# Kernel optimization log

Measured on AMD Instinct MI355X. Metric: run time of the kernel, lower is better.

Reference implementation:

```python
import jax, jax.numpy as jnp
import numpy as np

B, L, C = 16, 4000, 512
W = 5            # window_size == reduction
NH_G = 4         # int(8 * 0.5) grid-attention heads
NH_P = 4         # 8 - 4 pool-attention heads
DG = 256         # int(C * 0.5) grid inner dim
DP = 256         # int(C * (1 - 0.5)) pool inner dim
HD = 64          # head dim for both branches
EPS = 1e-5       # LayerNorm eps (torch default)


def setup_inputs() -> dict:
    key = jax.random.key(0)
    ks = jax.random.split(key, 8)
    s = 0.02
    return {
        "x": jax.random.normal(ks[0], (B, L, C), jnp.float32),
        # all linear weights stored [in, out] (torch Linear does x @ W.T)
        "gqkv_w": jax.random.normal(ks[1], (C, 3 * DG), jnp.float32) * s,
        "gqkv_b": jnp.zeros((3 * DG,), jnp.float32),
        "pq_w": jax.random.normal(ks[2], (C, DP), jnp.float32) * s,
        "pq_b": jnp.zeros((DP,), jnp.float32),
        "pkv_w": jax.random.normal(ks[3], (C, 2 * DP), jnp.float32) * s,
        "pkv_b": jnp.zeros((2 * DP,), jnp.float32),
        "conv_w": jax.random.normal(ks[4], (C, C), jnp.float32) * s,  # 1x1 Conv1d
        "conv_b": jnp.zeros((C,), jnp.float32),
        "ln_g": jnp.ones((C,), jnp.float32),
        "ln_b": jnp.zeros((C,), jnp.float32),
        "proj_w": jax.random.normal(ks[5], (C, C), jnp.float32) * s,
        "proj_b": jnp.zeros((C,), jnp.float32),
    }


def _mhsa(q, k, v, scale):
    # q,k,v: [b, h, n, hd]
    attn = jax.nn.softmax(jnp.einsum('bhqd,bhkd->bhqk', q, k) * scale, axis=-1)
    return jnp.einsum('bhqk,bhkd->bhqd', attn, v)


def reference(x, gqkv_w, gqkv_b, pq_w, pq_b, pkv_w, pkv_b,
              conv_w, conv_b, ln_g, ln_b, proj_w, proj_b):
    b, l, c = x.shape
    n = l // W
    scale = HD ** -0.5

    # ---- GridAttention (strided-window attention, ratio=0.5) ----
    # unfold: [b, l, c] -> [b*W, n, c] grouping tokens by residue mod W
    xg = x.reshape(b, n, W, c).transpose(0, 2, 1, 3).reshape(b * W, n, c)
    qkv = (xg @ gqkv_w + gqkv_b).reshape(b * W, n, 3, NH_G, HD).transpose(2, 0, 3, 1, 4)
    og = _mhsa(qkv[0], qkv[1], qkv[2], scale)               # [b*W, h, n, hd]
    og = og.transpose(0, 2, 1, 3).reshape(b, W, n, DG)       # back to [b, W, n, DG]
    og = og.transpose(0, 2, 1, 3).reshape(b, l, DG)          # fold -> [b, l, DG]

    # ---- PoolAttention (pooled KV, ratio=0.5) ----
    q = (x @ pq_w + pq_b).reshape(b, l, NH_P, HD).transpose(0, 2, 1, 3)
    pooled = x.reshape(b, n, W, c).mean(axis=2)              # AvgPool1d(k=5, s=5)
    pooled = pooled @ conv_w + conv_b                        # 1x1 Conv1d
    mu = pooled.mean(-1, keepdims=True)
    var = pooled.var(-1, keepdims=True)
    pooled = (pooled - mu) * jax.lax.rsqrt(var + EPS) * ln_g + ln_b
    pooled = jax.nn.gelu(pooled, approximate=False)          # torch GELU (erf)
    kv = (pooled @ pkv_w + pkv_b).reshape(b, n, 2, NH_P, HD).transpose(2, 0, 3, 1, 4)
    op = _mhsa(q, kv[0], kv[1], scale)                       # [b, h, l, hd]
    op = op.transpose(0, 2, 1, 3).reshape(b, l, DP)

    # ---- concat + output projection ----
    out = jnp.concatenate([og, op], axis=-1) @ proj_w + proj_b
    return out
```

## Files before the change

kernel.cpp:

```cpp
#include <hip/hip_runtime.h>
#include <hip/hip_bf16.h>
#include <math.h>

typedef short short8 __attribute__((ext_vector_type(8)));
typedef float f32x4 __attribute__((ext_vector_type(4)));

#define MFMA16(a, b, c) __builtin_amdgcn_mfma_f32_16x16x32_bf16((a), (b), (c), 0, 0, 0)
#define SM2 0.18033688f

#define BARRIER() { __builtin_amdgcn_sched_barrier(0); \
                    asm volatile("s_barrier" ::: "memory"); \
                    __builtin_amdgcn_sched_barrier(0); }
#define WAITVM(n) asm volatile("s_waitcnt vmcnt(" #n ")" ::: "memory")

__device__ __forceinline__ unsigned short f2bf(float f) {
  unsigned u = __builtin_bit_cast(unsigned, f);
  u += 0x7FFFu + ((u >> 16) & 1u);
  return (unsigned short)(u >> 16);
}
__device__ __forceinline__ float b2f(unsigned short h) {
  return __builtin_bit_cast(float, (unsigned)h << 16);
}
__device__ __forceinline__ unsigned cvtpk(float lo, float hi) {
  unsigned r;
  asm("v_cvt_pk_bf16_f32 %0, %1, %2" : "=v"(r) : "v"(lo), "v"(hi));
  return r;
}
__device__ __forceinline__ float vexp2(float x) {
  float r;
  asm("v_exp_f32 %0, %1" : "=v"(r) : "v"(x));
  return r;
}
__device__ __forceinline__ void gload16(const void* g, void* l) {
  __builtin_amdgcn_global_load_lds((const __attribute__((address_space(1))) unsigned*)g,
                                   (__attribute__((address_space(3))) unsigned*)l, 16, 0, 0);
}

__global__ __launch_bounds__(256) void cast_f32_bf16(const float* __restrict__ in,
                                                     unsigned short* __restrict__ out,
                                                     long n) {
  long i = ((long)blockIdx.x * 256 + threadIdx.x) * 4;
  if (i + 3 < n) {
    float4 v = *(const float4*)(in + i);
    ushort4 o;
    o.x = f2bf(v.x); o.y = f2bf(v.y); o.z = f2bf(v.z); o.w = f2bf(v.w);
    *(ushort4*)(out + i) = o;
  }
}

__global__ __launch_bounds__(256) void wtrans5(const float* __restrict__ w0,
                                               const float* __restrict__ w1,
                                               const float* __restrict__ w2,
                                               const float* __restrict__ w3,
                                               const float* __restrict__ w4,
                                               unsigned short* __restrict__ dst) {
  int seg = blockIdx.y;
  const float* src; int N; long doff;
  switch (seg) {
    case 0:  src = w0; N = 768; doff = 0;       break;
    case 1:  src = w1; N = 256; doff = 393216;  break;
    case 2:  src = w2; N = 512; doff = 524288;  break;
    case 3:  src = w3; N = 512; doff = 786432;  break;
    default: src = w4; N = 512; doff = 1048576; break;
  }
  int idx = blockIdx.x * 256 + threadIdx.x;
  if (idx < 512 * N) {
    int k = idx / N, n = idx - k * N;
    dst[doff + (long)n * 512 + k] = f2bf(src[idx]);
  }
}

__global__ __launch_bounds__(256) void pool_mean(const unsigned short* __restrict__ x,
                                                 unsigned short* __restrict__ pr) {
  long bi = blockIdx.x;
  const unsigned short* src = x + bi * 2560;
  int c = threadIdx.x * 2;
  float ax = 0.f, ay = 0.f;
#pragma unroll
  for (int w = 0; w < 5; ++w) {
    unsigned v = *(const unsigned*)(src + w * 512 + c);
    ax += b2f((unsigned short)(v & 0xffff));
    ay += b2f((unsigned short)(v >> 16));
  }
  unsigned out = (unsigned)f2bf(ax * 0.2f) | ((unsigned)f2bf(ay * 0.2f) << 16);
  *(unsigned*)(pr + bi * 512 + c) = out;
}

__global__ __launch_bounds__(256) void ln_gelu(const float* __restrict__ in,
                                               const float* __restrict__ g,
                                               const float* __restrict__ be,
                                               unsigned short* __restrict__ out) {
  long row = blockIdx.x;
  const float* src = in + row * 512;
  int tid = threadIdx.x;
  float2 v = *(const float2*)(src + tid * 2);
  float s = v.x + v.y, sq = v.x * v.x + v.y * v.y;
#pragma unroll
  for (int m = 1; m < 64; m <<= 1) {
    s  += __shfl_xor(s, m);
    sq += __shfl_xor(sq, m);
  }
  __shared__ float ss[4], ssq[4];
  int wv = tid >> 6;
  if ((tid & 63) == 0) { ss[wv] = s; ssq[wv] = sq; }
  __syncthreads();
  s  = ss[0] + ss[1] + ss[2] + ss[3];
  sq = ssq[0] + ssq[1] + ssq[2] + ssq[3];
  float mu = s * (1.0f / 512.0f);
  float var = sq * (1.0f / 512.0f) - mu * mu;
  float rs = rsqrtf(var + 1e-5f);
  int c = tid * 2;
#pragma unroll
  for (int e = 0; e < 2; ++e) {
    float xv = (e == 0 ? v.x : v.y);
    float y = (xv - mu) * rs * g[c + e] + be[c + e];
    float ge = 0.5f * y * (1.0f + erff(y * 0.70710678118654752f));
    out[row * 512 + c + e] = f2bf(ge);
  }
}

__global__ __launch_bounds__(256) void vtrans(const unsigned short* __restrict__ src,
                                              unsigned short* __restrict__ dst) {
  __shared__ unsigned short tile[64][64];
  int jt = blockIdx.x, s = blockIdx.y;
  int tid = threadIdx.x;
#pragma unroll
  for (int p = 0; p < 2; ++p) {
    int idx = p * 256 + tid;
    int j = idx >> 3, d8 = (idx & 7) * 8;
    int jg = min(jt * 64 + j, 799);
    short8 v = *(const short8*)(src + ((long)s * 800 + jg) * 64 + d8);
    *(short8*)&tile[j][d8] = v;
  }
  __syncthreads();
  int d = tid >> 2, jseg = (tid & 3) * 16;
  if (jt * 64 + jseg < 800) {
    short8 h0, h1;
#pragma unroll
    for (int i = 0; i < 8; ++i) { h0[i] = (short)tile[jseg + i][d]; h1[i] = (short)tile[jseg + 8 + i][d]; }
    unsigned short* o = dst + ((long)s * 64 + d) * 800 + jt * 64 + jseg;
    *(short8*)o = h0;
    *(short8*)(o + 8) = h1;
  }
}

__global__ __launch_bounds__(256) void gemm_bf16(const unsigned short* __restrict__ A,
                                                 const unsigned short* __restrict__ Bt,
                                                 const float* __restrict__ bias,
                                                 void* __restrict__ out0, void* __restrict__ out1,
                                                 int M, int N, int K, int gmode) {
  __shared__ unsigned short lA[2][128 * 32];
  __shared__ unsigned short lB[2][128 * 32];
  const int tid = threadIdx.x;
  const int lane = tid & 63, wv = tid >> 6;
  const int wr = wv >> 1, wc = wv & 1;
  const int l15 = lane & 15, lg = lane >> 4;

  const int nwg = gridDim.x * gridDim.y;
  const int bid = blockIdx.y * gridDim.x + blockIdx.x;
  const int w = (bid & 7) * (nwg >> 3) + (bid >> 3);
  const int m0 = (w / gridDim.x) * 128, n0 = (w % gridDim.x) * 128;

  const int r0  = tid >> 2;
  const int sw0 = ((tid & 3) * 16) ^ ((r0 & 3) << 4);
  const unsigned short* As0 = A  + (size_t)(m0 + r0)      * K + (sw0 >> 1);
  const unsigned short* As1 = A  + (size_t)(m0 + 64 + r0) * K + (sw0 >> 1);
  const unsigned short* Bs0 = Bt + (size_t)(n0 + r0)      * K + (sw0 >> 1);
  const unsigned short* Bs1 = Bt + (size_t)(n0 + 64 + r0) * K + (sw0 >> 1);

  f32x4 acc[4][4] = {};

#define GSTAGE(buf, k0)                                   \
  {                                                       \
    gload16(As0 + (k0), &lA[buf][wv * 512]);              \
    gload16(As1 + (k0), &lA[buf][2048 + wv * 512]);       \
    gload16(Bs0 + (k0), &lB[buf][wv * 512]);              \
    gload16(Bs1 + (k0), &lB[buf][2048 + wv * 512]);       \
  }

  const int nt = K >> 5;
  GSTAGE(0, 0);
  if (nt > 1) GSTAGE(1, 32);
  for (int t = 0; t < nt; ++t) {
    if (t + 1 < nt) { WAITVM(4); } else { WAITVM(0); }
    BARRIER();
    short8 af[4], bfr[4];
#pragma unroll
    for (int s2 = 0; s2 < 4; ++s2) {
      int ra = wr * 64 + s2 * 16 + l15;
      int rb = wc * 64 + s2 * 16 + l15;
      af[s2]  = *(const short8*)((char*)lA[t & 1] + ra * 64 + ((lg * 16) ^ ((ra & 3) << 4)));
      bfr[s2] = *(const short8*)((char*)lB[t & 1] + rb * 64 + ((lg * 16) ^ ((rb & 3) << 4)));
    }
#pragma unroll
    for (int i = 0; i < 4; ++i)
#pragma unroll
      for (int j = 0; j < 4; ++j)
        acc[i][j] = MFMA16(af[i], bfr[j], acc[i][j]);
    BARRIER();
    if (t + 2 < nt) GSTAGE(t & 1, (t + 2) * 32);
  }
#undef GSTAGE

#pragma unroll
  for (int i = 0; i < 4; ++i) {
#pragma unroll
    for (int r = 0; r < 4; ++r) {
      int row = m0 + wr * 64 + i * 16 + lg * 4 + r;
      long rg = 0;
      if (gmode == 3) {
        int b = row / 800, jj = row - b * 800;
        rg = (long)b * 204800 + (long)jj * 64;
      }
#pragma unroll
      for (int j = 0; j < 4; ++j) {
        int col = n0 + wc * 64 + j * 16 + l15;
        float vv = acc[i][j][r] + bias[col];
        if (gmode == 1) {
          ((float*)out0)[(size_t)row * N + col] = vv;
        } else {
          int hh = (col >> 6) & 3, d = col & 63;
          unsigned short* dst = (col < 256) ? (unsigned short*)out0 : (unsigned short*)out1;
          dst[rg + hh * 51200 + d] = f2bf(vv);
        }
      }
    }
  }
}

__global__ __launch_bounds__(512, 2) void gemm256(const unsigned short* __restrict__ A,
                                                  const unsigned short* __restrict__ Bt,
                                                  const float* __restrict__ bias,
                                                  const float* __restrict__ bias2,
                                                  void* __restrict__ out0, void* __restrict__ out1,
                                                  void* __restrict__ out2, void* __restrict__ out3,
                                                  int M, int N, int K, int gmode) {
  __shared__ char lds[131072];
  const int tid = threadIdx.x;
  const int lane = tid & 63, wv = tid >> 6;
  const int wr = wv >> 2, wc = wv & 3;
  const int l15 = lane & 15, lg = lane >> 4;

  const int nwg = gridDim.x * gridDim.y;
  const int bid = blockIdx.y * gridDim.x + blockIdx.x;
  const int q = nwg >> 3, r8 = nwg & 7;
  const int xcd = bid & 7, idx = bid >> 3;
  const int w = (xcd < r8 ? xcd * (q + 1) : r8 * (q + 1) + (xcd - r8) * q) + idx;
  const int m0 = (w / gridDim.x) * 256, n0 = (w % gridDim.x) * 256;

  const int srow = tid >> 3;
  const int scol = ((((lane & 7) ^ (lane >> 3)) << 4)) >> 1;
  const unsigned short* Ag[4];
  const unsigned short* Bg[4];
#pragma unroll
  for (int g = 0; g < 4; ++g) {
    Ag[g] = A  + (size_t)(m0 + g * 64 + srow) * K + scol;
    Bg[g] = Bt + (size_t)(n0 + g * 64 + srow) * K + scol;
  }

  f32x4 acc[8][4] = {};

#define GSTAGE2(buf, k0)                                                    \
  {                                                                         \
    _Pragma("unroll")                                                       \
    for (int g = 0; g < 4; ++g)                                             \
      gload16(Ag[g] + (k0), lds + (buf) * 32768 + g * 8192 + wv * 1024);    \
    _Pragma("unroll")                                                       \
    for (int g = 0; g < 4; ++g)                                             \
      gload16(Bg[g] + (k0), lds + 65536 + (buf) * 32768 + g * 8192 + wv * 1024); \
  }
#define RDA4(ibase, kk)                                             \
  _Pragma("unroll")                                                 \
  for (int i = 0; i < 4; ++i) {                                     \
    int ra = wr * 128 + ((ibase) + i) * 16 + l15;                   \
    af[i] = *(const short8*)(bufA + ra * 128 +                      \
             (((kk) * 64 + lg * 16) ^ ((ra & 7) << 4)));            \
  }
#define RDB4(kk)                                                    \
  _Pragma("unroll")                                                 \
  for (int j = 0; j < 4; ++j) {                                     \
    int rb = wc * 64 + j * 16 + l15;                                \
    bf[j] = *(const short8*)(bufB + rb * 128 +                      \
             (((kk) * 64 + lg * 16) ^ ((rb & 7) << 4)));            \
  }
#define PH_MFMA(ibase)                                              \
  __builtin_amdgcn_s_setprio(1);                                    \
  _Pragma("unroll")                                                 \
  for (int i = 0; i < 4; ++i)                                       \
    _Pragma("unroll")                                               \
    for (int j = 0; j < 4; ++j)                                     \
      acc[(ibase) + i][j] = MFMA16(af[i], bf[j], acc[(ibase) + i][j]); \
  __builtin_amdgcn_s_setprio(0);

  const int nt = K >> 6;
  GSTAGE2(0, 0);
  if (nt > 1) GSTAGE2(1, 64);
  for (int t = 0; t < nt; ++t) {
    if (t + 1 < nt) { WAITVM(8); } else { WAITVM(0); }
    BARRIER();
    const char* bufA = lds + (t & 1) * 32768;
    const char* bufB = lds + 65536 + (t & 1) * 32768;
    short8 af[4], bf[4];
    RDA4(0, 0); RDB4(0);
    BARRIER();
    PH_MFMA(0);
    BARRIER();
    RDA4(4, 0);
    BARRIER();
    PH_MFMA(4);
    BARRIER();
    RDA4(0, 1); RDB4(1);
    BARRIER();
    PH_MFMA(0);
    BARRIER();
    RDA4(4, 1);
    BARRIER();
    PH_MFMA(4);
    BARRIER();
    if (t + 2 < nt) GSTAGE2(t & 1, (t + 2) * 64);
  }
#undef GSTAGE2
#undef RDA4
#undef RDB4
#undef PH_MFMA

  float bb[4];
#pragma unroll
  for (int j = 0; j < 4; ++j) {
    int col = n0 + wc * 64 + j * 16 + l15;
    bb[j] = (gmode == 2 && col >= 768) ? bias2[col - 768] : bias[col];
  }
  const float qsc = (gmode == 2 && (n0 == 0 || n0 == 768)) ? SM2 : 1.0f;
  const int lwr = wr * 16 + lg * 4;
  const int lcol = wc * 64 + l15;
  const int lr_t = tid >> 4;
  const int c16 = (tid & 15) * 16;
  const int wrg = lr_t >> 4, rl = lr_t & 15;

  if (gmode == 1) {
    float* ls4 = (float*)lds;
#pragma unroll
    for (int i = 0; i < 8; ++i) {
      __syncthreads();
#pragma unroll
      for (int j = 0; j < 4; ++j)
#pragma unroll
        for (int rr = 0; rr < 4; ++rr)
          ls4[(lwr + rr) * 260 + lcol + j * 16] = acc[i][j][rr] + bb[j];
      __syncthreads();
      int gr = m0 + wrg * 128 + i * 16 + rl;
      float* dst = (float*)out0 + (size_t)gr * N + n0 + c16;
      const float* src = &ls4[lr_t * 260 + c16];
#pragma unroll
      for (int e = 0; e < 4; ++e)
        *(float4*)(dst + e * 4) = *(const float4*)(src + e * 4);
    }
  } else {
    unsigned short* ls2 = (unsigned short*)lds;
#pragma unroll
    for (int i = 0; i < 8; ++i) {
      __syncthreads();
#pragma unroll
      for (int j = 0; j < 4; ++j)
#pragma unroll
        for (int rr = 0; rr < 4; ++rr)
          ls2[(lwr + rr) * 264 + lcol + j * 16] = f2bf((acc[i][j][rr] + bb[j]) * qsc);
      __syncthreads();
      int gr = m0 + wrg * 128 + i * 16 + rl;
      unsigned short* dst;
      if (n0 == 768) {
        dst = (unsigned short*)out3 + (size_t)gr * 256 + c16;
      } else {
        int b = gr / 4000, l = gr - b * 4000;
        int jj = l / 5, ww = l - jj * 5;
        long rg = (long)(b * 5 + ww) * 204800 + (long)jj * 64;
        unsigned short* base = (n0 == 0) ? (unsigned short*)out0
                             : (n0 == 256) ? (unsigned short*)out1 : (unsigned short*)out2;
        dst = base + rg + (c16 >> 6) * 51200 + (c16 & 63);
      }
      const unsigned short* src = &ls2[lr_t * 264 + c16];
      *(uint4*)dst = *(const uint4*)src;
      *(uint4*)(dst + 8) = *(const uint4*)(src + 8);
    }
  }
}

__global__ __launch_bounds__(512) void flash_v7(const unsigned short* __restrict__ qg,
                                                const unsigned short* __restrict__ kg,
                                                const unsigned short* __restrict__ vtg,
                                                const unsigned short* __restrict__ qp,
                                                const unsigned short* __restrict__ kp,
                                                const unsigned short* __restrict__ vtp,
                                                unsigned short* __restrict__ cat) {
  __shared__ unsigned short lK[2][64 * 64];
  __shared__ unsigned short lV[2][64 * 64];
  __shared__ unsigned short lP[8][16 * 64];

  const int tid = threadIdx.x, lane = tid & 63, wv = tid >> 6;
  const int l15 = lane & 15, lg = lane >> 4;

  const int bid = blockIdx.x;
  const int w = (bid & 7) * 536 + (bid >> 3);
  int qt, sidx;
  const unsigned short *Kb, *Vb, *Qb;
  unsigned short* Ob;
  long qstr, ostr;
  int nq;
  if (w < 2240) {
    sidx = w / 7; qt = w - sidx * 7;
    Kb = kg + (long)sidx * 51200;
    Vb = vtg + (long)sidx * 51200;
    Qb = qg + (long)sidx * 51200; qstr = 64;
    int b = sidx / 20, rem = sidx % 20, ww = rem >> 2, h = rem & 3;
    Ob = cat + ((long)b * 4000 + ww) * 512 + h * 64; ostr = 2560;
    nq = 800;
  } else {
    int w2 = w - 2240;
    sidx = w2 >> 5; qt = w2 & 31;
    Kb = kp + (long)sidx * 51200;
    Vb = vtp + (long)sidx * 51200;
    int b = sidx >> 2, h = sidx & 3;
    Qb = qp + (long)b * 4000 * 256 + h * 64; qstr = 256;
    Ob = cat + (long)b * 4000 * 512 + 256 + h * 64; ostr = 512;
    nq = 4000;
  }

  int qrow = qt * 128 + wv * 16 + l15;
  int qrc = min(qrow, nq - 1);
  short8 q0 = *(const short8*)(Qb + (long)qrc * qstr + lg * 8);
  short8 q1 = *(const short8*)(Qb + (long)qrc * qstr + 32 + lg * 8);

  float ls = 0.f;
  f32x4 oacc[4] = {};

  const int srl = lane >> 3;
  const int swb = (((lane & 7) ^ srl) << 4);

#define FSTAGE(buf, t, CLAMP)                                                   \
  {                                                                             \
    int base = (t) * 64;                                                        \
    int krow = base + wv * 8 + srl;                                             \
    int vcol = base + (swb >> 1);                                               \
    if (CLAMP) { krow = min(krow, 799); vcol = min(vcol, 792); }                \
    gload16(Kb + (long)krow * 64 + (swb >> 1), &lK[buf][wv * 512]);             \
    gload16(Vb + (long)(wv * 8 + srl) * 800 + vcol, &lV[buf][wv * 512]);        \
  }

#define FTILE(buf)                                                              \
  {                                                                             \
    f32x4 st[4];                                                                \
    __builtin_amdgcn_s_setprio(1);                                              \
    _Pragma("unroll")                                                           \
    for (int ns = 0; ns < 4; ++ns) {                                            \
      int row = ns * 16 + l15;                                                  \
      short8 k0 = *(const short8*)((char*)lK[buf] + row * 128 +                 \
                                   ((lg * 16) ^ ((l15 & 7) << 4)));             \
      short8 k1 = *(const short8*)((char*)lK[buf] + row * 128 +                 \
                                   ((64 + lg * 16) ^ ((l15 & 7) << 4)));        \
      f32x4 z = {};                                                             \
      z = MFMA16(k0, q0, z);                                                    \
      z = MFMA16(k1, q1, z);                                                    \
      st[ns] = z;                                                               \
    }                                                                           \
    __builtin_amdgcn_s_setprio(0);                                              \
    float pv[16];                                                               \
    float lsl = 0.f;                                                            \
    _Pragma("unroll")                                                           \
    for (int ns = 0; ns < 4; ++ns)                                              \
      _Pragma("unroll")                                                         \
      for (int r = 0; r < 4; ++r) {                                             \
        float e = vexp2(st[ns][r]);                                             \
        pv[ns * 4 + r] = e;                                                     \
        lsl += e;                                                               \
      }                                                                         \
    ls += lsl;                                                                  \
    _Pragma("unroll")                                                           \
    for (int ns = 0; ns < 4; ++ns) {                                            \
      uint2 val;                                                                \
      val.x = cvtpk(pv[ns * 4 + 0], pv[ns * 4 + 1]);                            \
      val.y = cvtpk(pv[ns * 4 + 2], pv[ns * 4 + 3]);                            \
      *(uint2*)((char*)(&lP[wv][0]) + l15 * 128 +                               \
                ((ns * 32 + lg * 8) ^ ((l15 & 7) << 4))) = val;                 \
    }                                                                           \
    asm volatile("" ::: "memory");                                              \
    __builtin_amdgcn_s_setprio(1);                                              \
    _Pragma("unroll")                                                           \
    for (int half = 0; half < 2; ++half) {                                      \
      short8 pf = *(const short8*)((char*)(&lP[wv][0]) + l15 * 128 +            \
                                   ((half * 64 + lg * 16) ^ ((l15 & 7) << 4))); \
      _Pragma("unroll")                                                         \
      for (int ns2 = 0; ns2 < 4; ++ns2) {                                       \
        int row = ns2 * 16 + l15;                                               \
        short8 vf = *(const short8*)((char*)lV[buf] + row * 128 +               \
                                     ((half * 64 + lg * 16) ^ ((l15 & 7) << 4))); \
        oacc[ns2] = MFMA16(vf, pf, oacc[ns2]);                                  \
      }                                                                         \
    }                                                                           \
    __builtin_amdgcn_s_setprio(0);                                              \
  }

  FSTAGE(0, 0, 0);
  FSTAGE(1, 1, 0);
  for (int tb = 0; tb < 10; tb += 2) {
    WAITVM(2); BARRIER();
    FTILE(0);
    BARRIER();
    FSTAGE(0, tb + 2, 0);
    WAITVM(2); BARRIER();
    FTILE(1);
    BARRIER();
    FSTAGE(1, tb + 3, 0);
  }
  WAITVM(2); BARRIER();
  FTILE(0);
  BARRIER();
  FSTAGE(0, 12, 1);
  WAITVM(2); BARRIER();
  FTILE(1);
  BARRIER();
  WAITVM(0); BARRIER();
  {
    f32x4 st[2];
    __builtin_amdgcn_s_setprio(1);
#pragma unroll
    for (int ns = 0; ns < 2; ++ns) {
      int row = ns * 16 + l15;
      short8 k0 = *(const short8*)((char*)lK[0] + row * 128 +
                                   ((lg * 16) ^ ((l15 & 7) << 4)));
      short8 k1 = *(const short8*)((char*)lK[0] + row * 128 +
                                   ((64 + lg * 16) ^ ((l15 & 7) << 4)));
      f32x4 z = {};
      z = MFMA16(k0, q0, z);
      z = MFMA16(k1, q1, z);
      st[ns] = z;
    }
    __builtin_amdgcn_s_setprio(0);
    float pv[8];
    float lsl = 0.f;
#pragma unroll
    for (int ns = 0; ns < 2; ++ns)
#pragma unroll
      for (int r = 0; r < 4; ++r) {
        float e = vexp2(st[ns][r]);
        pv[ns * 4 + r] = e;
        lsl += e;
      }
    ls += lsl;
#pragma unroll
    for (int ns = 0; ns < 4; ++ns) {
      uint2 val;
      if (ns < 2) {
        val.x = cvtpk(pv[ns * 4 + 0], pv[ns * 4 + 1]);
        val.y = cvtpk(pv[ns * 4 + 2], pv[ns * 4 + 3]);
      } else {
        val.x = 0u; val.y = 0u;
      }
      *(uint2*)((char*)(&lP[wv][0]) + l15 * 128 +
                ((ns * 32 + lg * 8) ^ ((l15 & 7) << 4))) = val;
    }
    asm volatile("" ::: "memory");
    __builtin_amdgcn_s_setprio(1);
#pragma unroll
    for (int half = 0; half < 2; ++half) {
      short8 pf = *(const short8*)((char*)(&lP[wv][0]) + l15 * 128 +
                                   ((half * 64 + lg * 16) ^ ((l15 & 7) << 4)));
#pragma unroll
      for (int ns2 = 0; ns2 < 4; ++ns2) {
        int row = ns2 * 16 + l15;
        short8 vf = *(const short8*)((char*)lV[0] + row * 128 +
                                     ((half * 64 + lg * 16) ^ ((l15 & 7) << 4)));
        oacc[ns2] = MFMA16(vf, pf, oacc[ns2]);
      }
    }
    __builtin_amdgcn_s_setprio(0);
  }
#undef FSTAGE
#undef FTILE

  ls += __shfl_xor(ls, 16);
  ls += __shfl_xor(ls, 32);
  float inv = 1.0f / ls;

  __syncthreads();
  {
    int qrl = wv * 16 + l15;
#pragma unroll
    for (int ns2 = 0; ns2 < 4; ++ns2) {
      uint2 val;
      val.x = (unsigned)f2bf(oacc[ns2][0] * inv) | ((unsigned)f2bf(oacc[ns2][1] * inv) << 16);
      val.y = (unsigned)f2bf(oacc[ns2][2] * inv) | ((unsigned)f2bf(oacc[ns2][3] * inv) << 16);
      *(uint2*)((char*)lK + qrl * 128 + ((ns2 * 32 + lg * 8) ^ ((l15 & 7) << 4))) = val;
    }
  }
  __syncthreads();
#pragma unroll
  for (int p = 0; p < 2; ++p) {
    int o = (p * 512 + tid) * 16;
    int row = o >> 7, colb = o & 127;
    int qg2 = qt * 128 + row;
    if (qg2 < nq) {
      float4 v = *(const float4*)((char*)lK + (o & ~127) + (colb ^ ((row & 7) << 4)));
      *(float4*)(Ob + (long)qg2 * ostr + (colb >> 1)) = v;
    }
  }
}

extern "C" void kernel_launch(void* const* d_in, const int* in_sizes, int n_in,
                              void* d_out, int out_size, void* d_ws, size_t ws_size,
                              hipStream_t stream) {
  const float* x      = (const float*)d_in[0];
  const float* gqkv_w = (const float*)d_in[1];
  const float* gqkv_b = (const float*)d_in[2];
  const float* pq_w   = (const float*)d_in[3];
  const float* pq_b   = (const float*)d_in[4];
  const float* pkv_w  = (const float*)d_in[5];
  const float* pkv_b  = (const float*)d_in[6];
  const float* conv_w = (const float*)d_in[7];
  const float* conv_b = (const float*)d_in[8];
  const float* ln_g   = (const float*)d_in[9];
  const float* ln_b   = (const float*)d_in[10];
  const float* proj_w = (const float*)d_in[11];
  const float* proj_b = (const float*)d_in[12];

  char* ws = (char*)d_ws;
  unsigned short* xbf  = (unsigned short*)(ws + 0);
  unsigned short* cat  = xbf;
  unsigned short* qg   = (unsigned short*)(ws + 65536000);
  unsigned short* kg   = (unsigned short*)(ws + 98304000);
  unsigned short* vg   = (unsigned short*)(ws + 131072000);
  unsigned short* qp   = (unsigned short*)(ws + 163840000);
  unsigned short* pr   = (unsigned short*)(ws + 196608000);
  float*          cvt  = (float*)        (ws + 209715200);
  unsigned short* vtg  = (unsigned short*)(ws + 196608000);
  unsigned short* p2   = (unsigned short*)(ws + 235929600);
  unsigned short* vtp  = (unsigned short*)(ws + 235929600);
  unsigned short* kp   = (unsigned short*)(ws + 249036800);
  unsigned short* vp   = (unsigned short*)(ws + 255590400);
  unsigned short* wtg  = (unsigned short*)(ws + 262144000);
  unsigned short* wtkv = (unsigned short*)(ws + 263192576);
  unsigned short* wtc  = (unsigned short*)(ws + 263716864);
  unsigned short* wtp  = (unsigned short*)(ws + 264241152);

  cast_f32_bf16<<<32000, 256, 0, stream>>>(x, xbf, 64000L * 512);
  wtrans5<<<dim3(1536, 5), 256, 0, stream>>>(gqkv_w, pq_w, pkv_w, conv_w, proj_w, wtg);
  pool_mean<<<12800, 256, 0, stream>>>(xbf, pr);

  gemm_bf16<<<dim3(4, 100), 256, 0, stream>>>(pr, wtc, conv_b, cvt, nullptr,
                                              12800, 512, 512, 1);
  ln_gelu<<<12800, 256, 0, stream>>>(cvt, ln_g, ln_b, p2);
  gemm_bf16<<<dim3(4, 100), 256, 0, stream>>>(p2, wtkv, pkv_b, kp, vp,
                                              12800, 512, 512, 3);

  gemm256<<<dim3(4, 250), 512, 0, stream>>>(xbf, wtg, gqkv_b, pq_b,
                                            qg, kg, vg, qp,
                                            64000, 1024, 512, 2);

  vtrans<<<dim3(13, 320), 256, 0, stream>>>(vg, vtg);
  vtrans<<<dim3(13, 64), 256, 0, stream>>>(vp, vtp);

  flash_v7<<<4288, 512, 0, stream>>>(qg, kg, vtg, qp, kp, vtp, cat);

  gemm256<<<dim3(2, 250), 512, 0, stream>>>(cat, wtp, proj_b, nullptr,
                                            d_out, nullptr, nullptr, nullptr,
                                            64000, 512, 512, 1);
}
```

Before: 440.7 us.

## Load K/V fragments directly from global into registers in flash kernel

Drops the shared-memory double buffering of K and V tiles in the attention kernel. Each wave now loads its MFMA K and V fragments straight from global memory into registers, prefetching the next K tile while the current one is in use, and all block-wide barriers go away. The output epilogue now goes through each wave's private P buffer instead of a block-shared staging area, which removes the syncthreads there too. In exchange, every wave re-reads the same K/V tile from global memory (8x redundant, served by L1/L2), register pressure rises, and the V reads are less coalesced.

```diff
diff --git a/kernel.cpp b/kernel.cpp
--- a/kernel.cpp
+++ b/kernel.cpp
@@ -385,15 +385,13 @@
   }
 }
 
-__global__ __launch_bounds__(512) void flash_v7(const unsigned short* __restrict__ qg,
+__global__ __launch_bounds__(512) void flash_v8(const unsigned short* __restrict__ qg,
                                                 const unsigned short* __restrict__ kg,
                                                 const unsigned short* __restrict__ vtg,
                                                 const unsigned short* __restrict__ qp,
                                                 const unsigned short* __restrict__ kp,
                                                 const unsigned short* __restrict__ vtp,
                                                 unsigned short* __restrict__ cat) {
-  __shared__ unsigned short lK[2][64 * 64];
-  __shared__ unsigned short lV[2][64 * 64];
   __shared__ unsigned short lP[8][16 * 64];
 
   const int tid = threadIdx.x, lane = tid & 63, wv = tid >> 6;
@@ -433,112 +431,54 @@
   float ls = 0.f;
   f32x4 oacc[4] = {};
 
-  const int srl = lane >> 3;
-  const int swb = (((lane & 7) ^ srl) << 4);
-
-#define FSTAGE(buf, t, CLAMP)                                                   \
-  {                                                                             \
-    int base = (t) * 64;                                                        \
-    int krow = base + wv * 8 + srl;                                             \
-    int vcol = base + (swb >> 1);                                               \
-    if (CLAMP) { krow = min(krow, 799); vcol = min(vcol, 792); }                \
-    gload16(Kb + (long)krow * 64 + (swb >> 1), &lK[buf][wv * 512]);             \
-    gload16(Vb + (long)(wv * 8 + srl) * 800 + vcol, &lV[buf][wv * 512]);        \
-  }
-
-#define FTILE(buf)                                                              \
-  {                                                                             \
-    f32x4 st[4];                                                                \
-    __builtin_amdgcn_s_setprio(1);                                              \
-    _Pragma("unroll")                                                           \
-    for (int ns = 0; ns < 4; ++ns) {                                            \
-      int row = ns * 16 + l15;                                                  \
-      short8 k0 = *(const short8*)((char*)lK[buf] + row * 128 +                 \
-                                   ((lg * 16) ^ ((l15 & 7) << 4)));             \
-      short8 k1 = *(const short8*)((char*)lK[buf] + row * 128 +                 \
-                                   ((64 + lg * 16) ^ ((l15 & 7) << 4)));        \
-      f32x4 z = {};                                                             \
-      z = MFMA16(k0, q0, z);                                                    \
-      z = MFMA16(k1, q1, z);                                                    \
-      st[ns] = z;                                                               \
-    }                                                                           \
-    __builtin_amdgcn_s_setprio(0);                                              \
-    float pv[16];                                                               \
-    float lsl = 0.f;                                                            \
-    _Pragma("unroll")                                                           \
-    for (int ns = 0; ns < 4; ++ns)                                              \
-      _Pragma("unroll")                                                         \
-      for (int r = 0; r < 4; ++r) {                                             \
-        float e = vexp2(st[ns][r]);                                             \
-        pv[ns * 4 + r] = e;                                                     \
-        lsl += e;                                                               \
-      }                                                                         \
-    ls += lsl;                                                                  \
-    _Pragma("unroll")                                                           \
-    for (int ns = 0; ns < 4; ++ns) {                                            \
-      uint2 val;                                                                \
-      val.x = cvtpk(pv[ns * 4 + 0], pv[ns * 4 + 1]);                            \
-      val.y = cvtpk(pv[ns * 4 + 2], pv[ns * 4 + 3]);                            \
-      *(uint2*)((char*)(&lP[wv][0]) + l15 * 128 +                               \
-                ((ns * 32 + lg * 8) ^ ((l15 & 7) << 4))) = val;                 \
-    }                                                                           \
-    asm volatile("" ::: "memory");                                              \
-    __builtin_amdgcn_s_setprio(1);                                              \
-    _Pragma("unroll")                                                           \
-    for (int half = 0; half < 2; ++half) {                                      \
-      short8 pf = *(const short8*)((char*)(&lP[wv][0]) + l15 * 128 +            \
-                                   ((half * 64 + lg * 16) ^ ((l15 & 7) << 4))); \
-      _Pragma("unroll")                                                         \
-      for (int ns2 = 0; ns2 < 4; ++ns2) {                                       \
-        int row = ns2 * 16 + l15;                                               \
-        short8 vf = *(const short8*)((char*)lV[buf] + row * 128 +               \
-                                     ((half * 64 + lg * 16) ^ ((l15 & 7) << 4))); \
-        oacc[ns2] = MFMA16(vf, pf, oacc[ns2]);                                  \
-      }                                                                         \
-    }                                                                           \
-    __builtin_amdgcn_s_setprio(0);                                              \
-  }
-
-  FSTAGE(0, 0, 0);
-  FSTAGE(1, 1, 0);
-  for (int tb = 0; tb < 10; tb += 2) {
-    WAITVM(2); BARRIER();
-    FTILE(0);
-    BARRIER();
-    FSTAGE(0, tb + 2, 0);
-    WAITVM(2); BARRIER();
-    FTILE(1);
-    BARRIER();
-    FSTAGE(1, tb + 3, 0);
-  }
-  WAITVM(2); BARRIER();
-  FTILE(0);
-  BARRIER();
-  FSTAGE(0, 12, 1);
-  WAITVM(2); BARRIER();
-  FTILE(1);
-  BARRIER();
-  WAITVM(0); BARRIER();
-  {
-    f32x4 st[2];
+  const unsigned short* Kf = Kb + (long)l15 * 64 + lg * 8;
+  const unsigned short* Vf = Vb + (long)l15 * 800 + lg * 8;
+
+  short8 kf0[4], kf1[4];
+#pragma unroll
+  for (int ns = 0; ns < 4; ++ns) {
+    kf0[ns] = *(const short8*)(Kf + (long)ns * 16 * 64);
+    kf1[ns] = *(const short8*)(Kf + (long)ns * 16 * 64 + 32);
+  }
+
+  const int NT = 13;
+  for (int t = 0; t < NT - 1; ++t) {
+    short8 vf[2][4];
+#pragma unroll
+    for (int half = 0; half < 2; ++half)
+#pragma unroll
+      for (int ns2 = 0; ns2 < 4; ++ns2)
+        vf[half][ns2] = *(const short8*)(Vf + (long)ns2 * 16 * 800 + t * 64 + half * 32);
+
+    f32x4 st[4];
     __builtin_amdgcn_s_setprio(1);
 #pragma unroll
-    for (int ns = 0; ns < 2; ++ns) {
-      int row = ns * 16 + l15;
-      short8 k0 = *(const short8*)((char*)lK[0] + row * 128 +
-                                   ((lg * 16) ^ ((l15 & 7) << 4)));
-      short8 k1 = *(const short8*)((char*)lK[0] + row * 128 +
-                                   ((64 + lg * 16) ^ ((l15 & 7) << 4)));
+    for (int ns = 0; ns < 4; ++ns) {
       f32x4 z = {};
-      z = MFMA16(k0, q0, z);
-      z = MFMA16(k1, q1, z);
+      z = MFMA16(kf0[ns], q0, z);
+      z = MFMA16(kf1[ns], q1, z);
       st[ns] = z;
     }
     __builtin_amdgcn_s_setprio(0);
-    float pv[8];
+
+    if (t + 1 < 12) {
+#pragma unroll
+      for (int ns = 0; ns < 4; ++ns) {
+        kf0[ns] = *(const short8*)(Kf + (long)(t + 1) * 64 * 64 + (long)ns * 16 * 64);
+        kf1[ns] = *(const short8*)(Kf + (long)(t + 1) * 64 * 64 + (long)ns * 16 * 64 + 32);
+      }
+    } else {
+#pragma unroll
+      for (int ns = 0; ns < 2; ++ns) {
+        kf0[ns] = *(const short8*)(Kf + (long)12 * 64 * 64 + (long)ns * 16 * 64);
+        kf1[ns] = *(const short8*)(Kf + (long)12 * 64 * 64 + (long)ns * 16 * 64 + 32);
+      }
+    }
+
+    float pv[16];
     float lsl = 0.f;
 #pragma unroll
-    for (int ns = 0; ns < 2; ++ns)
+    for (int ns = 0; ns < 4; ++ns)
 #pragma unroll
       for (int r = 0; r < 4; ++r) {
         float e = vexp2(st[ns][r]);
@@ -549,58 +489,95 @@
 #pragma unroll
     for (int ns = 0; ns < 4; ++ns) {
       uint2 val;
-      if (ns < 2) {
-        val.x = cvtpk(pv[ns * 4 + 0], pv[ns * 4 + 1]);
-        val.y = cvtpk(pv[ns * 4 + 2], pv[ns * 4 + 3]);
-      } else {
-        val.x = 0u; val.y = 0u;
-      }
+      val.x = cvtpk(pv[ns * 4 + 0], pv[ns * 4 + 1]);
+      val.y = cvtpk(pv[ns * 4 + 2], pv[ns * 4 + 3]);
       *(uint2*)((char*)(&lP[wv][0]) + l15 * 128 +
                 ((ns * 32 + lg * 8) ^ ((l15 & 7) << 4))) = val;
     }
     asm volatile("" ::: "memory");
+
     __builtin_amdgcn_s_setprio(1);
 #pragma unroll
     for (int half = 0; half < 2; ++half) {
       short8 pf = *(const short8*)((char*)(&lP[wv][0]) + l15 * 128 +
                                    ((half * 64 + lg * 16) ^ ((l15 & 7) << 4)));
 #pragma unroll
-      for (int ns2 = 0; ns2 < 4; ++ns2) {
-        int row = ns2 * 16 + l15;
-        short8 vf = *(const short8*)((char*)lV[0] + row * 128 +
-                                     ((half * 64 + lg * 16) ^ ((l15 & 7) << 4)));
-        oacc[ns2] = MFMA16(vf, pf, oacc[ns2]);
-      }
+      for (int ns2 = 0; ns2 < 4; ++ns2)
+        oacc[ns2] = MFMA16(vf[half][ns2], pf, oacc[ns2]);
     }
     __builtin_amdgcn_s_setprio(0);
   }
-#undef FSTAGE
-#undef FTILE
+
+  {
+    short8 vf[4];
+#pragma unroll
+    for (int ns2 = 0; ns2 < 4; ++ns2)
+      vf[ns2] = *(const short8*)(Vf + (long)ns2 * 16 * 800 + 12 * 64);
+
+    f32x4 st[2];
+    __builtin_amdgcn_s_setprio(1);
+#pragma unroll
+    for (int ns = 0; ns < 2; ++ns) {
+      f32x4 z = {};
+      z = MFMA16(kf0[ns], q0, z);
+      z = MFMA16(kf1[ns], q1, z);
+      st[ns] = z;
+    }
+    __builtin_amdgcn_s_setprio(0);
+    float pv[8];
+    float lsl = 0.f;
+#pragma unroll
+    for (int ns = 0; ns < 2; ++ns)
+#pragma unroll
+      for (int r = 0; r < 4; ++r) {
+        float e = vexp2(st[ns][r]);
+        pv[ns * 4 + r] = e;
+        lsl += e;
+      }
+    ls += lsl;
+#pragma unroll
+    for (int ns = 0; ns < 2; ++ns) {
+      uint2 val;
+      val.x = cvtpk(pv[ns * 4 + 0], pv[ns * 4 + 1]);
+      val.y = cvtpk(pv[ns * 4 + 2], pv[ns * 4 + 3]);
+      *(uint2*)((char*)(&lP[wv][0]) + l15 * 128 +
+                ((ns * 32 + lg * 8) ^ ((l15 & 7) << 4))) = val;
+    }
+    asm volatile("" ::: "memory");
+    __builtin_amdgcn_s_setprio(1);
+    {
+      short8 pf = *(const short8*)((char*)(&lP[wv][0]) + l15 * 128 +
+                                   ((lg * 16) ^ ((l15 & 7) << 4)));
+#pragma unroll
+      for (int ns2 = 0; ns2 < 4; ++ns2)
+        oacc[ns2] = MFMA16(vf[ns2], pf, oacc[ns2]);
+    }
+    __builtin_amdgcn_s_setprio(0);
+  }
 
   ls += __shfl_xor(ls, 16);
   ls += __shfl_xor(ls, 32);
   float inv = 1.0f / ls;
 
-  __syncthreads();
   {
-    int qrl = wv * 16 + l15;
 #pragma unroll
     for (int ns2 = 0; ns2 < 4; ++ns2) {
       uint2 val;
       val.x = (unsigned)f2bf(oacc[ns2][0] * inv) | ((unsigned)f2bf(oacc[ns2][1] * inv) << 16);
       val.y = (unsigned)f2bf(oacc[ns2][2] * inv) | ((unsigned)f2bf(oacc[ns2][3] * inv) << 16);
-      *(uint2*)((char*)lK + qrl * 128 + ((ns2 * 32 + lg * 8) ^ ((l15 & 7) << 4))) = val;
-    }
-  }
-  __syncthreads();
-#pragma unroll
-  for (int p = 0; p < 2; ++p) {
-    int o = (p * 512 + tid) * 16;
-    int row = o >> 7, colb = o & 127;
-    int qg2 = qt * 128 + row;
-    if (qg2 < nq) {
-      float4 v = *(const float4*)((char*)lK + (o & ~127) + (colb ^ ((row & 7) << 4)));
-      *(float4*)(Ob + (long)qg2 * ostr + (colb >> 1)) = v;
+      *(uint2*)((char*)(&lP[wv][0]) + l15 * 128 +
+                ((ns2 * 32 + lg * 8) ^ ((l15 & 7) << 4))) = val;
+    }
+    asm volatile("" ::: "memory");
+#pragma unroll
+    for (int p = 0; p < 2; ++p) {
+      int r = p * 8 + (lane >> 3);
+      int cb = (lane & 7) * 16;
+      int qg2 = qt * 128 + wv * 16 + r;
+      if (qg2 < nq) {
+        float4 v = *(const float4*)((char*)(&lP[wv][0]) + r * 128 + (cb ^ ((r & 7) << 4)));
+        *(float4*)(Ob + (long)qg2 * ostr + (cb >> 1)) = v;
+      }
     }
   }
 }
@@ -658,7 +635,7 @@
   vtrans<<<dim3(13, 320), 256, 0, stream>>>(vg, vtg);
   vtrans<<<dim3(13, 64), 256, 0, stream>>>(vp, vtp);
 
-  flash_v7<<<4288, 512, 0, stream>>>(qg, kg, vtg, qp, kp, vtp, cat);
+  flash_v8<<<4288, 512, 0, stream>>>(qg, kg, vtg, qp, kp, vtp, cat);
 
   gemm256<<<dim3(2, 250), 512, 0, stream>>>(cat, wtp, proj_b, nullptr,
                                             d_out, nullptr, nullptr, nullptr,
```

After: 853.9 us. 93.7% more time.
